# Kernel tuning notes

Hardware: AMD Instinct MI355X
Metric: run time of the kernel (lower is better)

## Reference

```python
import jax, jax.numpy as jnp
import numpy as np

N_NODES = 50000
N_EDGES = 400000
N_GRAPHS = 512
IN_DIM = 768
HID = 64
BN_EPS = 1e-5


def setup_inputs() -> dict:
    key = jax.random.key(0)
    ks = jax.random.split(key, 12)
    x = jax.random.normal(ks[0], (N_NODES, IN_DIM), dtype=jnp.float32)
    edge_index = jax.random.randint(ks[1], (2, N_EDGES), 0, N_NODES, dtype=jnp.int64)
    batch = jnp.sort(jax.random.randint(ks[2], (N_NODES,), 0, N_GRAPHS, dtype=jnp.int64))

    def lin_init(k, fan_in, fan_out):
        kw, kb = jax.random.split(k)
        bound = 1.0 / np.sqrt(fan_in)
        W = jax.random.uniform(kw, (fan_in, fan_out), minval=-bound, maxval=bound, dtype=jnp.float32)
        b = jax.random.uniform(kb, (fan_out,), minval=-bound, maxval=bound, dtype=jnp.float32)
        return W, b

    w1a, b1a = lin_init(ks[3], IN_DIM, HID)
    w1b, b1b = lin_init(ks[4], HID, HID)
    w2a, b2a = lin_init(ks[5], HID, HID)
    w2b, b2b = lin_init(ks[6], HID, HID)
    wl, bl = lin_init(ks[7], 2 * HID, 2)

    ones = jnp.ones((HID,), jnp.float32)
    zeros = jnp.zeros((HID,), jnp.float32)
    return {
        "x": x, "edge_index": edge_index, "batch": batch,
        "w1a": w1a, "b1a": b1a, "g1": ones, "be1": zeros, "rm1": zeros, "rv1": ones,
        "w1b": w1b, "b1b": b1b,
        "w2a": w2a, "b2a": b2a, "g2": ones, "be2": zeros, "rm2": zeros, "rv2": ones,
        "w2b": w2b, "b2b": b2b,
        "wl": wl, "bl": bl,
    }


def _bn_eval(h, gamma, beta, rm, rv):
    # BatchNorm1d in eval mode: normalize with running stats
    return (h - rm) * (gamma * jax.lax.rsqrt(rv + BN_EPS)) + beta


def _gin_conv(x, src, dst, Wa, ba, gamma, beta, rm, rv, Wb, bb):
    # GINConv eps=0: h = MLP(x + sum_{j in N(i)} x_j); messages x[src] scatter-added to dst
    agg = jax.ops.segment_sum(x[src], dst, num_segments=N_NODES)
    h = x + agg
    h = jnp.dot(h, Wa) + ba
    h = jax.nn.relu(_bn_eval(h, gamma, beta, rm, rv))
    return jnp.dot(h, Wb) + bb


def reference(x, edge_index, batch,
              w1a, b1a, g1, be1, rm1, rv1, w1b, b1b,
              w2a, b2a, g2, be2, rm2, rv2, w2b, b2b,
              wl, bl):
    src, dst = edge_index[0], edge_index[1]
    # eval mode: dropout_edge and F.dropout are identity
    x1 = jax.nn.relu(_gin_conv(x, src, dst, w1a, b1a, g1, be1, rm1, rv1, w1b, b1b))
    x2 = jax.nn.relu(_gin_conv(x1, src, dst, w2a, b2a, g2, be2, rm2, rv2, w2b, b2b))
    x_jk = jnp.concatenate([x1, x2], axis=-1)  # [N, 2*HID]
    x_pool = jax.ops.segment_sum(x_jk, batch, num_segments=N_GRAPHS)  # [G, 2*HID]
    return jnp.dot(x_pool, wl) + bl  # [G, 2]
```

## Files before the change

### kernel.cpp

```cpp
#include <hip/hip_runtime.h>

constexpr int N_NODES  = 50000;
constexpr int N_EDGES  = 400000;
constexpr int N_GRAPHS = 512;
constexpr int IN_DIM   = 768;
constexpr int HID      = 64;
constexpr float BN_EPS = 1e-5f;
constexpr int CAP      = 64;

typedef __attribute__((ext_vector_type(8))) short bf16x8;
typedef __attribute__((ext_vector_type(4))) float f32x4;

__device__ __forceinline__ float bf2f(ushort u) {
  return __uint_as_float((unsigned int)u << 16);
}
__device__ __forceinline__ ushort f2bf(float f) {
  unsigned int u = __float_as_uint(f);
  u = (u + 0x7fff + ((u >> 16) & 1)) >> 16;
  return (ushort)u;
}

constexpr int W1A_E = HID * IN_DIM;
constexpr int WB_E  = HID * HID;
__global__ __launch_bounds__(256) void convert_all(
    const float* __restrict__ w1a, const float* __restrict__ w1b,
    const float* __restrict__ w2a, const float* __restrict__ w2b,
    const float* __restrict__ bl,
    ushort* __restrict__ WT, ushort* __restrict__ WT1b,
    ushort* __restrict__ WT2a, ushort* __restrict__ WT2b,
    float* __restrict__ out, int* __restrict__ cnt) {
  int i = blockIdx.x * 256 + threadIdx.x;
  if (i < W1A_E) {
    int c = i / IN_DIM, k = i - c * IN_DIM;
    WT[i] = f2bf(w1a[(size_t)k * HID + c]);
    return;
  }
  int j = i - W1A_E;
  if (j < 3 * WB_E) {
    int w = j / WB_E, r = j - w * WB_E;
    int c = r / HID, k = r - c * HID;
    const float* W = (w == 0) ? w1b : (w == 1) ? w2a : w2b;
    ushort* D = (w == 0) ? WT1b : (w == 1) ? WT2a : WT2b;
    D[r] = f2bf(W[(size_t)k * HID + c]);
    return;
  }
  int o = j - 3 * WB_E;
  if (o < N_GRAPHS * 2) { out[o] = bl[o & 1]; return; }
  int z = o - N_GRAPHS * 2;
  if (z < N_NODES) cnt[z] = 0;
}

__global__ __launch_bounds__(256) void gemm_in_mfma(const float* __restrict__ X,
                                                    const ushort* __restrict__ WT,
                                                    ushort* __restrict__ P) {
  __shared__ ushort xs[64][64];
  __shared__ ushort ws[64][64];
  const int tid  = threadIdx.x;
  const int row0 = blockIdx.x * 64;
  const int wave = tid >> 6;
  const int lane = tid & 63;
  const int quad = lane >> 4;
  const int l16  = lane & 15;

  const int srow = tid >> 2;
  const int sk   = (tid & 3) * 16;
  const int ch0  = ((sk >> 3) + 0) ^ (srow & 7);
  const int ch1  = ((sk >> 3) + 1) ^ (srow & 7);

  int gr = row0 + srow;
  gr = gr < N_NODES ? gr : N_NODES - 1;
  const float*  xrow = &X[(size_t)gr * IN_DIM + sk];
  const ushort* wrow = &WT[(size_t)srow * IN_DIM + sk];

  f32x4 acc[4] = {};

  float4 xv0 = *(const float4*)&xrow[0];
  float4 xv1 = *(const float4*)&xrow[4];
  float4 xv2 = *(const float4*)&xrow[8];
  float4 xv3 = *(const float4*)&xrow[12];
  uint4  wv0 = *(const uint4*)&wrow[0];
  uint4  wv1 = *(const uint4*)&wrow[8];

  for (int kt = 0; kt < IN_DIM; kt += 64) {
    ushort xb[16];
    {
      float xv[16] = {xv0.x, xv0.y, xv0.z, xv0.w, xv1.x, xv1.y, xv1.z, xv1.w,
                      xv2.x, xv2.y, xv2.z, xv2.w, xv3.x, xv3.y, xv3.z, xv3.w};
#pragma unroll
      for (int i = 0; i < 16; i++) xb[i] = f2bf(xv[i]);
    }
    *(uint4*)&xs[srow][ch0 * 8] = *(uint4*)&xb[0];
    *(uint4*)&xs[srow][ch1 * 8] = *(uint4*)&xb[8];
    *(uint4*)&ws[srow][ch0 * 8] = wv0;
    *(uint4*)&ws[srow][ch1 * 8] = wv1;
    __syncthreads();

    if (kt + 64 < IN_DIM) {
      xv0 = *(const float4*)&xrow[kt + 64 + 0];
      xv1 = *(const float4*)&xrow[kt + 64 + 4];
      xv2 = *(const float4*)&xrow[kt + 64 + 8];
      xv3 = *(const float4*)&xrow[kt + 64 + 12];
      wv0 = *(const uint4*)&wrow[kt + 64 + 0];
      wv1 = *(const uint4*)&wrow[kt + 64 + 8];
    }

    const int ar   = wave * 16 + l16;
    const int axor = ar & 7;
#pragma unroll
    for (int ks = 0; ks < 2; ks++) {
      bf16x8 a = *(const bf16x8*)&xs[ar][((ks * 4 + quad) ^ axor) * 8];
#pragma unroll
      for (int ct = 0; ct < 4; ct++) {
        const int br = ct * 16 + l16;
        bf16x8 b = *(const bf16x8*)&ws[br][((ks * 4 + quad) ^ (br & 7)) * 8];
        acc[ct] = __builtin_amdgcn_mfma_f32_16x16x32_bf16(a, b, acc[ct], 0, 0, 0);
      }
    }
    __syncthreads();
  }

#pragma unroll
  for (int ct = 0; ct < 4; ct++) {
#pragma unroll
    for (int r = 0; r < 4; r++) {
      int row = row0 + wave * 16 + quad * 4 + r;
      if (row < N_NODES) P[(size_t)row * HID + ct * 16 + l16] = f2bf(acc[ct][r]);
    }
  }
}

__global__ __launch_bounds__(256) void build_buckets(const int* __restrict__ src,
                                                     const int* __restrict__ dst,
                                                     int* __restrict__ cnt,
                                                     int* __restrict__ bucket) {
  int e = blockIdx.x * 256 + threadIdx.x;
  if (e >= N_EDGES) return;
  int s = src[e];
  int d = dst[e];
  int slot = atomicAdd(&cnt[d], 1);
  if (slot < CAP) bucket[d * CAP + slot] = s;
}

template <int CHAIN>
__global__ __launch_bounds__(256) void fused_mlp(
    const int* __restrict__ cnt, const int* __restrict__ bucket,
    const ushort* __restrict__ Pin,
    const float* __restrict__ bin, const float* __restrict__ g,
    const float* __restrict__ be, const float* __restrict__ rm,
    const float* __restrict__ rv,
    const ushort* __restrict__ WT1, const float* __restrict__ b1,
    const ushort* __restrict__ WT2,
    ushort* __restrict__ OUT1, ushort* __restrict__ OUT2) {
  __shared__ ushort xs[64][64];
  __shared__ ushort ws[64][64];
  __shared__ ushort ws2[64][64];
  __shared__ float sS[64], sT[64];
  const int tid  = threadIdx.x;
  const int row0 = blockIdx.x * 64;
  const int srow = tid >> 2;
  const int sub  = tid & 3;
  const int qc0  = sub * 2;

  if (tid < 64) {
    float s = g[tid] * rsqrtf(rv[tid] + BN_EPS);
    sS[tid] = s;
    sT[tid] = (bin[tid] - rm[tid]) * s + be[tid];
  }
  {
    uint4 w0 = *(const uint4*)&WT1[(size_t)srow * HID + qc0 * 8];
    uint4 w1 = *(const uint4*)&WT1[(size_t)srow * HID + qc0 * 8 + 8];
    *(uint4*)&ws[srow][((qc0 + 0) ^ (srow & 7)) * 8] = w0;
    *(uint4*)&ws[srow][((qc0 + 1) ^ (srow & 7)) * 8] = w1;
    if (CHAIN) {
      uint4 v0 = *(const uint4*)&WT2[(size_t)srow * HID + qc0 * 8];
      uint4 v1 = *(const uint4*)&WT2[(size_t)srow * HID + qc0 * 8 + 8];
      *(uint4*)&ws2[srow][((qc0 + 0) ^ (srow & 7)) * 8] = v0;
      *(uint4*)&ws2[srow][((qc0 + 1) ^ (srow & 7)) * 8] = v1;
    }
  }
  __syncthreads();

  {
    int node = row0 + srow;
    node = node < N_NODES ? node : N_NODES - 1;
    float acc[16];
    {
      ushort b0[16];
      const ushort* base = &Pin[(size_t)node * HID + sub * 16];
      *(uint4*)&b0[0] = *(const uint4*)&base[0];
      *(uint4*)&b0[8] = *(const uint4*)&base[8];
#pragma unroll
      for (int j = 0; j < 16; j++) acc[j] = bf2f(b0[j]);
    }
    int c = cnt[node];
    c = c < CAP ? c : CAP;
    const int* bkt = &bucket[node * CAP];
    int i = 0;
    for (; i + 4 <= c; i += 4) {
      int4 s4 = *(const int4*)&bkt[i];
      ushort r0[16], r1[16], r2[16], r3[16];
      const ushort* p0 = &Pin[(size_t)s4.x * HID + sub * 16];
      const ushort* p1 = &Pin[(size_t)s4.y * HID + sub * 16];
      const ushort* p2 = &Pin[(size_t)s4.z * HID + sub * 16];
      const ushort* p3 = &Pin[(size_t)s4.w * HID + sub * 16];
      *(uint4*)&r0[0] = *(const uint4*)&p0[0]; *(uint4*)&r0[8] = *(const uint4*)&p0[8];
      *(uint4*)&r1[0] = *(const uint4*)&p1[0]; *(uint4*)&r1[8] = *(const uint4*)&p1[8];
      *(uint4*)&r2[0] = *(const uint4*)&p2[0]; *(uint4*)&r2[8] = *(const uint4*)&p2[8];
      *(uint4*)&r3[0] = *(const uint4*)&p3[0]; *(uint4*)&r3[8] = *(const uint4*)&p3[8];
#pragma unroll
      for (int j = 0; j < 16; j++)
        acc[j] += (bf2f(r0[j]) + bf2f(r1[j])) + (bf2f(r2[j]) + bf2f(r3[j]));
    }
    for (; i < c; i++) {
      const ushort* p0 = &Pin[(size_t)bkt[i] * HID + sub * 16];
      ushort r0[16];
      *(uint4*)&r0[0] = *(const uint4*)&p0[0]; *(uint4*)&r0[8] = *(const uint4*)&p0[8];
#pragma unroll
      for (int j = 0; j < 16; j++) acc[j] += bf2f(r0[j]);
    }
    ushort hb[16];
#pragma unroll
    for (int j = 0; j < 16; j++) {
      int col = sub * 16 + j;
      float v = fmaxf(fmaf(acc[j], sS[col], sT[col]), 0.0f);
      hb[j] = f2bf(v);
    }
    *(uint4*)&xs[srow][((qc0 + 0) ^ (srow & 7)) * 8] = *(uint4*)&hb[0];
    *(uint4*)&xs[srow][((qc0 + 1) ^ (srow & 7)) * 8] = *(uint4*)&hb[8];
  }
  __syncthreads();

  const int wave = tid >> 6, lane = tid & 63, quad = lane >> 4, l16 = lane & 15;
  const int ar = wave * 16 + l16, axor = ar & 7;

  f32x4 acc1[4] = {};
#pragma unroll
  for (int ks = 0; ks < 2; ks++) {
    bf16x8 a = *(const bf16x8*)&xs[ar][((ks * 4 + quad) ^ axor) * 8];
#pragma unroll
    for (int ct = 0; ct < 4; ct++) {
      const int br = ct * 16 + l16;
      bf16x8 b = *(const bf16x8*)&ws[br][((ks * 4 + quad) ^ (br & 7)) * 8];
      acc1[ct] = __builtin_amdgcn_mfma_f32_16x16x32_bf16(a, b, acc1[ct], 0, 0, 0);
    }
  }

  if (CHAIN) __syncthreads();

  ushort hv[4][4];
#pragma unroll
  for (int ct = 0; ct < 4; ct++) {
    const int col = ct * 16 + l16;
    const float bo = b1[col];
#pragma unroll
    for (int r = 0; r < 4; r++) {
      int lrow = wave * 16 + quad * 4 + r;
      int grow = row0 + lrow;
      float v = fmaxf(acc1[ct][r] + bo, 0.0f);
      ushort h = f2bf(v);
      hv[ct][r] = h;
      if (grow < N_NODES) OUT1[(size_t)grow * HID + col] = h;
    }
  }

  if (CHAIN) {
#pragma unroll
    for (int ct = 0; ct < 4; ct++) {
      const int col = ct * 16 + l16;
#pragma unroll
      for (int r = 0; r < 4; r++) {
        int lrow = wave * 16 + quad * 4 + r;
        xs[lrow][(((col >> 3) ^ (lrow & 7)) * 8) + (col & 7)] = hv[ct][r];
      }
    }
    __syncthreads();

    f32x4 acc2[4] = {};
#pragma unroll
    for (int ks = 0; ks < 2; ks++) {
      bf16x8 a = *(const bf16x8*)&xs[ar][((ks * 4 + quad) ^ axor) * 8];
#pragma unroll
      for (int ct = 0; ct < 4; ct++) {
        const int br = ct * 16 + l16;
        bf16x8 b = *(const bf16x8*)&ws2[br][((ks * 4 + quad) ^ (br & 7)) * 8];
        acc2[ct] = __builtin_amdgcn_mfma_f32_16x16x32_bf16(a, b, acc2[ct], 0, 0, 0);
      }
    }
#pragma unroll
    for (int ct = 0; ct < 4; ct++) {
      const int col = ct * 16 + l16;
#pragma unroll
      for (int r = 0; r < 4; r++) {
        int grow = row0 + wave * 16 + quad * 4 + r;
        if (grow < N_NODES) OUT2[(size_t)grow * HID + col] = f2bf(acc2[ct][r]);
      }
    }
  }
}

__global__ __launch_bounds__(256) void pool2(const ushort* __restrict__ x1,
                                             const ushort* __restrict__ x2,
                                             const int* __restrict__ batch,
                                             const float* __restrict__ wl,
                                             float* __restrict__ out) {
  __shared__ float gacc[N_GRAPHS * 2];
  __shared__ float wl_s[2 * HID * 2];
  const int tid = threadIdx.x;
#pragma unroll
  for (int i = tid; i < N_GRAPHS * 2; i += 256) gacc[i] = 0.0f;
  wl_s[tid] = wl[tid];
  __syncthreads();

  const int wave = tid >> 6, lane = tid & 63;
  const int sub = lane & 3, noff = lane >> 2;
  const int nbase = blockIdx.x * 256 + wave * 64;
#pragma unroll
  for (int it = 0; it < 4; it++) {
    int node = nbase + it * 16 + noff;
    bool ok = node < N_NODES;
    int cn = ok ? node : N_NODES - 1;
    ushort v1[16], v2[16];
    const ushort* r1 = &x1[(size_t)cn * HID + sub * 16];
    const ushort* r2 = &x2[(size_t)cn * HID + sub * 16];
    *(uint4*)&v1[0] = *(const uint4*)&r1[0];
    *(uint4*)&v1[8] = *(const uint4*)&r1[8];
    *(uint4*)&v2[0] = *(const uint4*)&r2[0];
    *(uint4*)&v2[8] = *(const uint4*)&r2[8];
    float p0 = 0.0f, p1 = 0.0f;
#pragma unroll
    for (int j = 0; j < 16; j++) {
      int e = sub * 16 + j;
      float a = bf2f(v1[j]);
      float b = bf2f(v2[j]);
      p0 += a * wl_s[e * 2 + 0] + b * wl_s[(HID + e) * 2 + 0];
      p1 += a * wl_s[e * 2 + 1] + b * wl_s[(HID + e) * 2 + 1];
    }
    p0 += __shfl_xor(p0, 1); p0 += __shfl_xor(p0, 2);
    p1 += __shfl_xor(p1, 1); p1 += __shfl_xor(p1, 2);
    if (sub == 0 && ok) {
      int gr = batch[node];
      atomicAdd(&gacc[gr * 2 + 0], p0);
      atomicAdd(&gacc[gr * 2 + 1], p1);
    }
  }
  __syncthreads();
#pragma unroll
  for (int i = tid; i < N_GRAPHS * 2; i += 256) {
    float v = gacc[i];
    if (v != 0.0f) atomicAdd(&out[i], v);
  }
}

extern "C" void kernel_launch(void* const* d_in, const int* in_sizes, int n_in,
                              void* d_out, int out_size, void* d_ws, size_t ws_size,
                              hipStream_t stream) {
  const float* x   = (const float*)d_in[0];
  const int*   ei  = (const int*)d_in[1];
  const int*   bat = (const int*)d_in[2];
  const float* w1a = (const float*)d_in[3];
  const float* b1a = (const float*)d_in[4];
  const float* g1  = (const float*)d_in[5];
  const float* be1 = (const float*)d_in[6];
  const float* rm1 = (const float*)d_in[7];
  const float* rv1 = (const float*)d_in[8];
  const float* w1b = (const float*)d_in[9];
  const float* b1b = (const float*)d_in[10];
  const float* w2a = (const float*)d_in[11];
  const float* b2a = (const float*)d_in[12];
  const float* g2  = (const float*)d_in[13];
  const float* be2 = (const float*)d_in[14];
  const float* rm2 = (const float*)d_in[15];
  const float* rv2 = (const float*)d_in[16];
  const float* w2b = (const float*)d_in[17];
  const float* b2b = (const float*)d_in[18];
  const float* wl  = (const float*)d_in[19];
  const float* bl  = (const float*)d_in[20];
  float* out = (float*)d_out;

  const int* src = ei;
  const int* dst = ei + N_EDGES;

  const size_t FB = (size_t)N_NODES * HID;
  ushort* P1   = (ushort*)d_ws;
  ushort* P2   = P1 + FB;
  ushort* X1   = P2 + FB;
  ushort* X2   = X1 + FB;
  ushort* WT   = X2 + FB;
  ushort* WT1b = WT + (size_t)W1A_E;
  ushort* WT2a = WT1b + WB_E;
  ushort* WT2b = WT2a + WB_E;
  int* cnt     = (int*)(WT2b + WB_E);
  int* bucket  = cnt + N_NODES;

  const int GB = (N_NODES + 63) / 64;
  const int BB = (N_EDGES + 255) / 256;
  const int PB = (N_NODES + 255) / 256;
  const int CB = (W1A_E + 3 * WB_E + N_GRAPHS * 2 + N_NODES + 255) / 256;

  convert_all<<<CB, 256, 0, stream>>>(w1a, w1b, w2a, w2b, bl,
                                      WT, WT1b, WT2a, WT2b, out, cnt);
  build_buckets<<<BB, 256, 0, stream>>>(src, dst, cnt, bucket);

  gemm_in_mfma<<<GB, 256, 0, stream>>>(x, WT, P1);
  fused_mlp<1><<<GB, 256, 0, stream>>>(cnt, bucket, P1, b1a, g1, be1, rm1, rv1,
                                       WT1b, b1b, WT2a, X1, P2);
  fused_mlp<0><<<GB, 256, 0, stream>>>(cnt, bucket, P2, b2a, g2, be2, rm2, rv2,
                                       WT2b, b2b, nullptr, X2, nullptr);
  pool2<<<PB, 256, 0, stream>>>(X1, X2, bat, wl, out);
}
```

Baseline: 334.3 us.

## Fuse graph pooling into MLP kernels and widen input GEMM tile to 128 rows

Removes the separate pool kernel and the X1/X2 intermediate writes by projecting each layer's ReLU output onto its half of the final linear weights inside fused_mlp. The per-node scalars are reduced with shuffles and accumulated into per-graph shared-memory bins, which are then atomically added to the output. The input GEMM now processes 128 rows per block with two accumulator sets, so each weight tile is reused across more rows. The cost is a larger shared-memory footprint and a per-block gacc clear and flush in every fused_mlp block, which adds global atomics.

```diff
diff --git a/kernel.cpp b/kernel.cpp
--- a/kernel.cpp
+++ b/kernel.cpp
@@ -53,80 +53,79 @@
 __global__ __launch_bounds__(256) void gemm_in_mfma(const float* __restrict__ X,
                                                     const ushort* __restrict__ WT,
                                                     ushort* __restrict__ P) {
-  __shared__ ushort xs[64][64];
+  __shared__ ushort xs[128][64];
   __shared__ ushort ws[64][64];
   const int tid  = threadIdx.x;
-  const int row0 = blockIdx.x * 64;
-  const int wave = tid >> 6;
-  const int lane = tid & 63;
-  const int quad = lane >> 4;
-  const int l16  = lane & 15;
-
-  const int srow = tid >> 2;
-  const int sk   = (tid & 3) * 16;
-  const int ch0  = ((sk >> 3) + 0) ^ (srow & 7);
-  const int ch1  = ((sk >> 3) + 1) ^ (srow & 7);
-
+  const int row0 = blockIdx.x * 128;
+  const int wave = tid >> 6, lane = tid & 63, quad = lane >> 4, l16 = lane & 15;
+
+  const int srow = tid >> 1;
+  const int sk   = (tid & 1) * 32;
   int gr = row0 + srow;
   gr = gr < N_NODES ? gr : N_NODES - 1;
-  const float*  xrow = &X[(size_t)gr * IN_DIM + sk];
-  const ushort* wrow = &WT[(size_t)srow * IN_DIM + sk];
-
-  f32x4 acc[4] = {};
-
-  float4 xv0 = *(const float4*)&xrow[0];
-  float4 xv1 = *(const float4*)&xrow[4];
-  float4 xv2 = *(const float4*)&xrow[8];
-  float4 xv3 = *(const float4*)&xrow[12];
-  uint4  wv0 = *(const uint4*)&wrow[0];
-  uint4  wv1 = *(const uint4*)&wrow[8];
+  const float* xrow = &X[(size_t)gr * IN_DIM + sk];
+  const int wrow = tid >> 2;
+  const int wc0  = (tid & 3) * 2;
+  const ushort* wrp = &WT[(size_t)wrow * IN_DIM + wc0 * 8];
+
+  f32x4 acc[2][4] = {};
+
+  float4 xv[8];
+#pragma unroll
+  for (int i = 0; i < 8; i++) xv[i] = *(const float4*)&xrow[i * 4];
+  uint4 wv0 = *(const uint4*)&wrp[0];
+  uint4 wv1 = *(const uint4*)&wrp[8];
 
   for (int kt = 0; kt < IN_DIM; kt += 64) {
-    ushort xb[16];
-    {
-      float xv[16] = {xv0.x, xv0.y, xv0.z, xv0.w, xv1.x, xv1.y, xv1.z, xv1.w,
-                      xv2.x, xv2.y, xv2.z, xv2.w, xv3.x, xv3.y, xv3.z, xv3.w};
-#pragma unroll
-      for (int i = 0; i < 16; i++) xb[i] = f2bf(xv[i]);
-    }
-    *(uint4*)&xs[srow][ch0 * 8] = *(uint4*)&xb[0];
-    *(uint4*)&xs[srow][ch1 * 8] = *(uint4*)&xb[8];
-    *(uint4*)&ws[srow][ch0 * 8] = wv0;
-    *(uint4*)&ws[srow][ch1 * 8] = wv1;
+    ushort xb[32];
+#pragma unroll
+    for (int i = 0; i < 8; i++) {
+      xb[i * 4 + 0] = f2bf(xv[i].x);
+      xb[i * 4 + 1] = f2bf(xv[i].y);
+      xb[i * 4 + 2] = f2bf(xv[i].z);
+      xb[i * 4 + 3] = f2bf(xv[i].w);
+    }
+#pragma unroll
+    for (int j = 0; j < 4; j++)
+      *(uint4*)&xs[srow][(((sk >> 3) + j) ^ (srow & 7)) * 8] = *(uint4*)&xb[j * 8];
+    *(uint4*)&ws[wrow][((wc0 + 0) ^ (wrow & 7)) * 8] = wv0;
+    *(uint4*)&ws[wrow][((wc0 + 1) ^ (wrow & 7)) * 8] = wv1;
     __syncthreads();
 
     if (kt + 64 < IN_DIM) {
-      xv0 = *(const float4*)&xrow[kt + 64 + 0];
-      xv1 = *(const float4*)&xrow[kt + 64 + 4];
-      xv2 = *(const float4*)&xrow[kt + 64 + 8];
-      xv3 = *(const float4*)&xrow[kt + 64 + 12];
-      wv0 = *(const uint4*)&wrow[kt + 64 + 0];
-      wv1 = *(const uint4*)&wrow[kt + 64 + 8];
-    }
-
-    const int ar   = wave * 16 + l16;
-    const int axor = ar & 7;
+#pragma unroll
+      for (int i = 0; i < 8; i++) xv[i] = *(const float4*)&xrow[kt + 64 + i * 4];
+      wv0 = *(const uint4*)&wrp[kt + 64];
+      wv1 = *(const uint4*)&wrp[kt + 64 + 8];
+    }
+
+    const int ar0 = wave * 32 + l16;
+    const int ar1 = ar0 + 16;
 #pragma unroll
     for (int ks = 0; ks < 2; ks++) {
-      bf16x8 a = *(const bf16x8*)&xs[ar][((ks * 4 + quad) ^ axor) * 8];
+      bf16x8 a0 = *(const bf16x8*)&xs[ar0][((ks * 4 + quad) ^ (ar0 & 7)) * 8];
+      bf16x8 a1 = *(const bf16x8*)&xs[ar1][((ks * 4 + quad) ^ (ar1 & 7)) * 8];
 #pragma unroll
       for (int ct = 0; ct < 4; ct++) {
         const int br = ct * 16 + l16;
         bf16x8 b = *(const bf16x8*)&ws[br][((ks * 4 + quad) ^ (br & 7)) * 8];
-        acc[ct] = __builtin_amdgcn_mfma_f32_16x16x32_bf16(a, b, acc[ct], 0, 0, 0);
+        acc[0][ct] = __builtin_amdgcn_mfma_f32_16x16x32_bf16(a0, b, acc[0][ct], 0, 0, 0);
+        acc[1][ct] = __builtin_amdgcn_mfma_f32_16x16x32_bf16(a1, b, acc[1][ct], 0, 0, 0);
       }
     }
     __syncthreads();
   }
 
 #pragma unroll
-  for (int ct = 0; ct < 4; ct++) {
-#pragma unroll
-    for (int r = 0; r < 4; r++) {
-      int row = row0 + wave * 16 + quad * 4 + r;
-      if (row < N_NODES) P[(size_t)row * HID + ct * 16 + l16] = f2bf(acc[ct][r]);
-    }
-  }
+  for (int g2 = 0; g2 < 2; g2++)
+#pragma unroll
+    for (int ct = 0; ct < 4; ct++)
+#pragma unroll
+      for (int r = 0; r < 4; r++) {
+        int row = row0 + wave * 32 + g2 * 16 + quad * 4 + r;
+        if (row < N_NODES)
+          P[(size_t)row * HID + ct * 16 + l16] = f2bf(acc[g2][ct][r]);
+      }
 }
 
 __global__ __launch_bounds__(256) void build_buckets(const int* __restrict__ src,
@@ -149,18 +148,24 @@
     const float* __restrict__ be, const float* __restrict__ rm,
     const float* __restrict__ rv,
     const ushort* __restrict__ WT1, const float* __restrict__ b1,
-    const ushort* __restrict__ WT2,
-    ushort* __restrict__ OUT1, ushort* __restrict__ OUT2) {
+    const ushort* __restrict__ WT2, ushort* __restrict__ OUT2,
+    const int* __restrict__ batch, const float* __restrict__ wlh,
+    float* __restrict__ out) {
   __shared__ ushort xs[64][64];
   __shared__ ushort ws[64][64];
-  __shared__ ushort ws2[64][64];
+  __shared__ ushort ws2[CHAIN ? 64 : 1][64];
   __shared__ float sS[64], sT[64];
+  __shared__ float gacc[N_GRAPHS * 2];
+  __shared__ float wl_s[2 * HID];
   const int tid  = threadIdx.x;
   const int row0 = blockIdx.x * 64;
   const int srow = tid >> 2;
   const int sub  = tid & 3;
   const int qc0  = sub * 2;
 
+#pragma unroll
+  for (int i = tid; i < N_GRAPHS * 2; i += 256) gacc[i] = 0.0f;
+  if (tid < 2 * HID) wl_s[tid] = wlh[tid];
   if (tid < 64) {
     float s = g[tid] * rsqrtf(rv[tid] + BN_EPS);
     sS[tid] = s;
@@ -247,30 +252,55 @@
 
   if (CHAIN) __syncthreads();
 
-  ushort hv[4][4];
+  float v[4][4];
 #pragma unroll
   for (int ct = 0; ct < 4; ct++) {
-    const int col = ct * 16 + l16;
-    const float bo = b1[col];
-#pragma unroll
-    for (int r = 0; r < 4; r++) {
-      int lrow = wave * 16 + quad * 4 + r;
-      int grow = row0 + lrow;
-      float v = fmaxf(acc1[ct][r] + bo, 0.0f);
-      ushort h = f2bf(v);
-      hv[ct][r] = h;
-      if (grow < N_NODES) OUT1[(size_t)grow * HID + col] = h;
-    }
-  }
-
-  if (CHAIN) {
+    const float bo = b1[ct * 16 + l16];
+#pragma unroll
+    for (int r = 0; r < 4; r++) v[ct][r] = fmaxf(acc1[ct][r] + bo, 0.0f);
+  }
+
+  {
+    float p0[4] = {}, p1[4] = {};
 #pragma unroll
     for (int ct = 0; ct < 4; ct++) {
       const int col = ct * 16 + l16;
+      const float w0 = wl_s[col * 2 + 0], w1 = wl_s[col * 2 + 1];
+#pragma unroll
+      for (int r = 0; r < 4; r++) {
+        p0[r] = fmaf(v[ct][r], w0, p0[r]);
+        p1[r] = fmaf(v[ct][r], w1, p1[r]);
+      }
+    }
+#pragma unroll
+    for (int m = 1; m < 16; m <<= 1) {
+#pragma unroll
+      for (int r = 0; r < 4; r++) {
+        p0[r] += __shfl_xor(p0[r], m);
+        p1[r] += __shfl_xor(p1[r], m);
+      }
+    }
+    if (l16 == 0) {
+#pragma unroll
+      for (int r = 0; r < 4; r++) {
+        int node = row0 + wave * 16 + quad * 4 + r;
+        if (node < N_NODES) {
+          int gi = batch[node];
+          atomicAdd(&gacc[gi * 2 + 0], p0[r]);
+          atomicAdd(&gacc[gi * 2 + 1], p1[r]);
+        }
+      }
+    }
+  }
+
+  if (CHAIN) {
+#pragma unroll
+    for (int ct = 0; ct < 4; ct++) {
+      const int col = ct * 16 + l16;
 #pragma unroll
       for (int r = 0; r < 4; r++) {
         int lrow = wave * 16 + quad * 4 + r;
-        xs[lrow][(((col >> 3) ^ (lrow & 7)) * 8) + (col & 7)] = hv[ct][r];
+        xs[lrow][(((col >> 3) ^ (lrow & 7)) * 8) + (col & 7)] = f2bf(v[ct][r]);
       }
     }
     __syncthreads();
@@ -296,58 +326,12 @@
       }
     }
   }
-}
-
-__global__ __launch_bounds__(256) void pool2(const ushort* __restrict__ x1,
-                                             const ushort* __restrict__ x2,
-                                             const int* __restrict__ batch,
-                                             const float* __restrict__ wl,
-                                             float* __restrict__ out) {
-  __shared__ float gacc[N_GRAPHS * 2];
-  __shared__ float wl_s[2 * HID * 2];
-  const int tid = threadIdx.x;
-#pragma unroll
-  for (int i = tid; i < N_GRAPHS * 2; i += 256) gacc[i] = 0.0f;
-  wl_s[tid] = wl[tid];
+
   __syncthreads();
-
-  const int wave = tid >> 6, lane = tid & 63;
-  const int sub = lane & 3, noff = lane >> 2;
-  const int nbase = blockIdx.x * 256 + wave * 64;
-#pragma unroll
-  for (int it = 0; it < 4; it++) {
-    int node = nbase + it * 16 + noff;
-    bool ok = node < N_NODES;
-    int cn = ok ? node : N_NODES - 1;
-    ushort v1[16], v2[16];
-    const ushort* r1 = &x1[(size_t)cn * HID + sub * 16];
-    const ushort* r2 = &x2[(size_t)cn * HID + sub * 16];
-    *(uint4*)&v1[0] = *(const uint4*)&r1[0];
-    *(uint4*)&v1[8] = *(const uint4*)&r1[8];
-    *(uint4*)&v2[0] = *(const uint4*)&r2[0];
-    *(uint4*)&v2[8] = *(const uint4*)&r2[8];
-    float p0 = 0.0f, p1 = 0.0f;
-#pragma unroll
-    for (int j = 0; j < 16; j++) {
-      int e = sub * 16 + j;
-      float a = bf2f(v1[j]);
-      float b = bf2f(v2[j]);
-      p0 += a * wl_s[e * 2 + 0] + b * wl_s[(HID + e) * 2 + 0];
-      p1 += a * wl_s[e * 2 + 1] + b * wl_s[(HID + e) * 2 + 1];
-    }
-    p0 += __shfl_xor(p0, 1); p0 += __shfl_xor(p0, 2);
-    p1 += __shfl_xor(p1, 1); p1 += __shfl_xor(p1, 2);
-    if (sub == 0 && ok) {
-      int gr = batch[node];
-      atomicAdd(&gacc[gr * 2 + 0], p0);
-      atomicAdd(&gacc[gr * 2 + 1], p1);
-    }
-  }
-  __syncthreads();
 #pragma unroll
   for (int i = tid; i < N_GRAPHS * 2; i += 256) {
-    float v = gacc[i];
-    if (v != 0.0f) atomicAdd(&out[i], v);
+    float vv = gacc[i];
+    if (vv != 0.0f) atomicAdd(&out[i], vv);
   }
 }
 
@@ -383,28 +367,26 @@
   const size_t FB = (size_t)N_NODES * HID;
   ushort* P1   = (ushort*)d_ws;
   ushort* P2   = P1 + FB;
-  ushort* X1   = P2 + FB;
-  ushort* X2   = X1 + FB;
-  ushort* WT   = X2 + FB;
+  ushort* WT   = P2 + FB;
   ushort* WT1b = WT + (size_t)W1A_E;
   ushort* WT2a = WT1b + WB_E;
   ushort* WT2b = WT2a + WB_E;
   int* cnt     = (int*)(WT2b + WB_E);
   int* bucket  = cnt + N_NODES;
 
-  const int GB = (N_NODES + 63) / 64;
-  const int BB = (N_EDGES + 255) / 256;
-  const int PB = (N_NODES + 255) / 256;
-  const int CB = (W1A_E + 3 * WB_E + N_GRAPHS * 2 + N_NODES + 255) / 256;
+  const int GB1 = (N_NODES + 127) / 128;
+  const int GBF = (N_NODES + 63) / 64;
+  const int BB  = (N_EDGES + 255) / 256;
+  const int CB  = (W1A_E + 3 * WB_E + N_GRAPHS * 2 + N_NODES + 255) / 256;
 
   convert_all<<<CB, 256, 0, stream>>>(w1a, w1b, w2a, w2b, bl,
                                       WT, WT1b, WT2a, WT2b, out, cnt);
   build_buckets<<<BB, 256, 0, stream>>>(src, dst, cnt, bucket);
 
-  gemm_in_mfma<<<GB, 256, 0, stream>>>(x, WT, P1);
-  fused_mlp<1><<<GB, 256, 0, stream>>>(cnt, bucket, P1, b1a, g1, be1, rm1, rv1,
-                                       WT1b, b1b, WT2a, X1, P2);
-  fused_mlp<0><<<GB, 256, 0, stream>>>(cnt, bucket, P2, b2a, g2, be2, rm2, rv2,
-                                       WT2b, b2b, nullptr, X2, nullptr);
-  pool2<<<PB, 256, 0, stream>>>(X1, X2, bat, wl, out);
-}
+  gemm_in_mfma<<<GB1, 256, 0, stream>>>(x, WT, P1);
+  fused_mlp<1><<<GBF, 256, 0, stream>>>(cnt, bucket, P1, b1a, g1, be1, rm1, rv1,
+                                        WT1b, b1b, WT2a, P2, bat, wl, out);
+  fused_mlp<0><<<GBF, 256, 0, stream>>>(cnt, bucket, P2, b2a, g2, be2, rm2, rv2,
+                                        WT2b, b2b, nullptr, nullptr, bat,
+                                        wl + 2 * HID, out);
+}
```

After: 328.2 us. About the same (-1.8%).
